# Kernel optimization log

Hardware: AMD Instinct MI355X
Metric: run time of the kernel (lower is better)

Reference implementation:

```python
import jax, jax.numpy as jnp
import numpy as np

THRESHOLD = 0.5
NEG_POS_RATIO = 3
CONF_WEIGHT = 1.0
VAR = (0.1, 0.1, 0.2, 0.2)
EPS_LOG = 1e-5


def _center_to_corner(p):
    cx, cy, w, h = p[:, 0], p[:, 1], p[:, 2], p[:, 3]
    return jnp.stack([cx - w / 2, cy - h / 2, cx + w / 2, cy + h / 2], axis=1)


def _iou(gt, pr):  # gt [M,4] corners, pr [P,4] corners -> [M,P]
    lt = jnp.maximum(gt[:, None, :2], pr[None, :, :2])
    rb = jnp.minimum(gt[:, None, 2:], pr[None, :, 2:])
    wh = jnp.clip(rb - lt, 0.0)
    inter = wh[..., 0] * wh[..., 1]
    area_g = (gt[:, 2] - gt[:, 0]) * (gt[:, 3] - gt[:, 1])
    area_p = (pr[:, 2] - pr[:, 0]) * (pr[:, 3] - pr[:, 1])
    return inter / (area_g[:, None] + area_p[None, :] - inter + 1e-10)


def _match_one(gt_boxes, priors_corner):
    # standard SSD matching: per-prior best GT if IoU >= threshold, else -1;
    # each GT additionally claims its best prior.
    iou = _iou(gt_boxes, priors_corner)            # [M,P]
    best_gt = jnp.argmax(iou, axis=0)              # [P]
    best_iou = jnp.max(iou, axis=0)                # [P]
    truth = jnp.where(best_iou >= THRESHOLD, best_gt, -1)
    best_prior = jnp.argmax(iou, axis=1)           # [M]
    truth = truth.at[best_prior].set(jnp.arange(gt_boxes.shape[0]))
    return truth


def _encode(matched_gt, priors):
    # matched_gt [B,P,4] corners, priors [P,4] center form -> [B,P,4]
    g_cx = (matched_gt[..., 0] + matched_gt[..., 2]) / 2
    g_cy = (matched_gt[..., 1] + matched_gt[..., 3]) / 2
    g_w = matched_gt[..., 2] - matched_gt[..., 0]
    g_h = matched_gt[..., 3] - matched_gt[..., 1]
    p_cx, p_cy, p_w, p_h = priors[:, 0], priors[:, 1], priors[:, 2], priors[:, 3]
    enc_cx = (g_cx - p_cx) / (p_w * VAR[0])
    enc_cy = (g_cy - p_cy) / (p_h * VAR[1])
    enc_w = jnp.log(g_w / p_w + EPS_LOG) / VAR[2]
    enc_h = jnp.log(g_h / p_h + EPS_LOG) / VAR[3]
    return jnp.stack([enc_cx, enc_cy, enc_w, enc_h], axis=-1)


def setup_inputs() -> dict:
    key = jax.random.key(0)
    ks = jax.random.split(key, 7)
    B, P, C, M = 64, 8732, 81, 20
    pred_loc = jax.random.normal(ks[0], (B, P, 4), jnp.float32)
    pred_conf = jax.random.normal(ks[1], (B, P, C), jnp.float32)
    # priors in center form (cx, cy, w, h)
    p_c = jax.random.uniform(ks[2], (P, 2), jnp.float32)
    p_wh = jax.random.uniform(ks[3], (P, 2), jnp.float32, minval=0.05, maxval=0.5)
    priors = jnp.concatenate([p_c, p_wh], axis=1)
    # GT boxes in corner form, guaranteed valid (x2>x1, y2>y1)
    g_c = jax.random.uniform(ks[4], (B, M, 2), jnp.float32, minval=0.2, maxval=0.8)
    g_wh = jax.random.uniform(ks[5], (B, M, 2), jnp.float32, minval=0.05, maxval=0.3)
    targets_boxes = jnp.concatenate([g_c - g_wh / 2, g_c + g_wh / 2], axis=-1)
    targets_labels = jax.random.randint(ks[6], (B, M), 1, C, jnp.int32)
    return {"pred_loc": pred_loc, "pred_conf": pred_conf, "priors": priors,
            "targets_boxes": targets_boxes, "targets_labels": targets_labels}


def reference(pred_loc, pred_conf, priors, targets_boxes, targets_labels):
    B, P, C = pred_conf.shape
    priors_corner = _center_to_corner(priors)
    truth = jax.vmap(lambda g: _match_one(g, priors_corner))(targets_boxes)  # [B,P]
    pos_mask = truth != -1
    safe = jnp.maximum(truth, 0)
    matched_gt = jax.vmap(lambda t, s: t[s])(targets_boxes, safe)            # [B,P,4]
    target_conf = jnp.where(pos_mask,
                            jax.vmap(lambda l, s: l[s])(targets_labels, safe), 0)

    # localization loss: smooth-L1 (beta=1), sum over matched priors, / batch
    enc = _encode(matched_gt, priors)
    d = pred_loc - enc
    ad = jnp.abs(d)
    sl1 = jnp.where(ad < 1.0, 0.5 * d * d, ad - 0.5)
    loc_loss = jnp.sum(sl1 * pos_mask[..., None]) / B

    # confidence loss with hard negative mining (3:1, double-argsort rank trick)
    logp = jax.nn.log_softmax(pred_conf, axis=-1)                            # [B,P,C]
    ce = -jnp.take_along_axis(logp, target_conf[..., None], axis=-1)[..., 0]  # [B,P]
    ce_neg = jnp.where(pos_mask, 0.0, ce)
    order = jnp.argsort(-ce_neg, axis=1)
    rank = jnp.argsort(order, axis=1)
    pos_num = jnp.sum(pos_mask, axis=1, keepdims=True)
    neg_num = jnp.minimum(NEG_POS_RATIO * pos_num, P - 1)
    neg_mask = rank < neg_num
    prior_mask = pos_mask | neg_mask
    conf_loss = jnp.sum(ce * prior_mask) / jnp.sum(prior_mask) / B * CONF_WEIGHT
    return (loc_loss, conf_loss)
```

## Files before the change

kernel.cpp:

```cpp
#include <hip/hip_runtime.h>
#include <hip/hip_bf16.h>

#define B_   64
#define P_   8732
#define C_   81
#define M_   20
#define BP_  (B_*P_)
#define NCH  9
#define CER  64
#define SBLK 1024

__global__ __launch_bounds__(256) void iou_kernel(
    const float* __restrict__ priors, const float* __restrict__ tboxes,
    int* __restrict__ truth, unsigned long long* __restrict__ bestc,
    int* __restrict__ pos_cnt, float* __restrict__ pos_sum,
    float* __restrict__ accums, int* __restrict__ done)
{
    const int b = blockIdx.y;
    const int tid = threadIdx.x;

    if (blockIdx.x == 0 && b == 0) {
        if (tid < B_) { pos_cnt[tid] = 0; pos_sum[tid] = 0.f; }
        if (tid >= B_ && tid < B_ + 3) accums[tid - B_] = 0.f;
        if (tid == B_ + 3) *done = 0;
    }

    __shared__ float s_gt[M_][4];
    __shared__ float s_ga[M_];
    __shared__ float s_red[M_][4];
    __shared__ int   s_redp[M_][4];

    if (tid < M_*4) ((float*)s_gt)[tid] = tboxes[b*M_*4 + tid];
    __syncthreads();
    if (tid < M_) s_ga[tid] = (s_gt[tid][2]-s_gt[tid][0]) * (s_gt[tid][3]-s_gt[tid][1]);
    __syncthreads();

    float lb[M_]; int lp[M_];
    #pragma unroll
    for (int m=0;m<M_;++m){ lb[m] = -1.0f; lp[m] = 0x7FFFFFFF; }

    const float4* pr4 = (const float4*)priors;
    const int p0 = blockIdx.x * 1024;
    const int pend = min(p0 + 1024, P_);
    for (int p = p0 + tid; p < pend; p += 256) {
        float4 pc = pr4[p];
        float px0 = pc.x - pc.z*0.5f, py0 = pc.y - pc.w*0.5f;
        float px1 = pc.x + pc.z*0.5f, py1 = pc.y + pc.w*0.5f;
        float pa = pc.z * pc.w;
        float best = -1.0f; int bg = 0;
        #pragma unroll
        for (int m=0;m<M_;++m){
            float ix0 = fmaxf(s_gt[m][0], px0);
            float iy0 = fmaxf(s_gt[m][1], py0);
            float ix1 = fminf(s_gt[m][2], px1);
            float iy1 = fminf(s_gt[m][3], py1);
            float iw = fmaxf(ix1-ix0, 0.f), ih = fmaxf(iy1-iy0, 0.f);
            float inter = iw*ih;
            float iou = inter / (s_ga[m] + pa - inter + 1e-10f);
            if (iou > best) { best = iou; bg = m; }
            if (iou > lb[m]) { lb[m] = iou; lp[m] = p; }
        }
        truth[(size_t)b*P_ + p] = (best >= 0.5f) ? bg : -1;
    }

    const int lane = tid & 63, wid = tid >> 6;
    #pragma unroll
    for (int m=0;m<M_;++m){
        float v = lb[m]; int ip = lp[m];
        for (int off=32; off; off>>=1){
            float ov = __shfl_down(v, off); int op = __shfl_down(ip, off);
            if (ov > v || (ov == v && op < ip)) { v = ov; ip = op; }
        }
        if (lane == 0) { s_red[m][wid] = v; s_redp[m][wid] = ip; }
    }
    __syncthreads();
    if (tid < M_) {
        const int m = tid;
        float v = s_red[m][0]; int ip = s_redp[m][0];
        for (int w=1; w<4; ++w){
            float ov = s_red[m][w]; int op = s_redp[m][w];
            if (ov > v || (ov == v && op < ip)) { v = ov; ip = op; }
        }
        bestc[(b*M_ + m)*NCH + blockIdx.x] =
            ((unsigned long long)__float_as_uint(v) << 32) | (unsigned)(P_ - 1 - ip);
    }
}

__global__ __launch_bounds__(256) void ce_loc_kernel(
    const float* __restrict__ pred_conf, const float* __restrict__ pred_loc,
    const float* __restrict__ priors, const float* __restrict__ tboxes,
    const int* __restrict__ tlabels, const int* __restrict__ truth,
    const unsigned long long* __restrict__ bestc,
    float* __restrict__ ce_neg, int* __restrict__ pos_cnt,
    float* __restrict__ pos_sum, float* __restrict__ accums)
{
    __shared__ int   s_fp[2][M_];
    __shared__ int   s_pos[2];
    __shared__ float s_psum[2];
    __shared__ float s_loc[4];
    const int tid = threadIdx.x;
    const int base = blockIdx.x * CER;
    const int b0 = base / P_;

    if (tid < 2*M_) {
        const int j = tid / M_, m = tid - j*M_;
        const int bb = b0 + j;
        int p = -1;
        if (bb < B_) {
            const unsigned long long* src = &bestc[(bb*M_ + m)*NCH];
            unsigned long long best = src[0];
            #pragma unroll
            for (int c = 1; c < NCH; ++c) { unsigned long long kk = src[c]; if (kk > best) best = kk; }
            p = P_ - 1 - (int)(unsigned)(best & 0xFFFFFFFFu);
        }
        s_fp[j][m] = p;
    }
    if (tid < 2) { s_pos[tid] = 0; s_psum[tid] = 0.f; }
    __syncthreads();

    const int r = tid >> 2;
    const int q = tid & 3;
    const int bp = base + r;
    const int b  = bp / P_;
    const int p  = bp - b * P_;
    const int jb = b - b0;
    const float* row = pred_conf + (size_t)bp * C_;

    float v[21];
    #pragma unroll
    for (int i = 0; i < 21; ++i) {
        const int c = q + 4*i;
        v[i] = (c < C_) ? row[c] : -1e30f;
    }
    float mx = v[0];
    #pragma unroll
    for (int i = 1; i < 21; ++i) mx = fmaxf(mx, v[i]);
    mx = fmaxf(mx, __shfl_xor(mx, 1));
    mx = fmaxf(mx, __shfl_xor(mx, 2));
    float s = 0.f;
    #pragma unroll
    for (int i = 0; i < 21; ++i) s += __expf(v[i] - mx);
    s += __shfl_xor(s, 1);
    s += __shfl_xor(s, 2);

    float locacc = 0.f;
    if (q == 0) {
        int t = truth[bp];
        #pragma unroll
        for (int m = 0; m < M_; ++m)
            if (s_fp[jb][m] == p) t = m;
        const int cls = (t >= 0) ? tlabels[b*M_ + t] : 0;
        const float ce = mx + __logf(s) - row[cls];
        if (t >= 0) {
            atomicAdd(&s_pos[jb], 1);
            atomicAdd(&s_psum[jb], ce);
            ce_neg[bp] = 0.f;
            float4 pc = ((const float4*)priors)[p];
            float4 g  = ((const float4*)tboxes)[b*M_ + t];
            float gcx = (g.x+g.z)*0.5f, gcy = (g.y+g.w)*0.5f;
            float gw = g.z - g.x, gh = g.w - g.y;
            float e0 = (gcx - pc.x) / (pc.z * 0.1f);
            float e1 = (gcy - pc.y) / (pc.w * 0.1f);
            float e2 = __logf(gw / pc.z + 1e-5f) * 5.0f;
            float e3 = __logf(gh / pc.w + 1e-5f) * 5.0f;
            float4 pl = ((const float4*)pred_loc)[bp];
            float d0 = pl.x-e0, d1 = pl.y-e1, d2 = pl.z-e2, d3 = pl.w-e3;
            float a0 = fabsf(d0), a1 = fabsf(d1), a2 = fabsf(d2), a3 = fabsf(d3);
            locacc = (a0<1.f ? 0.5f*d0*d0 : a0-0.5f)
                   + (a1<1.f ? 0.5f*d1*d1 : a1-0.5f)
                   + (a2<1.f ? 0.5f*d2*d2 : a2-0.5f)
                   + (a3<1.f ? 0.5f*d3*d3 : a3-0.5f);
        } else {
            ce_neg[bp] = ce;
        }
    }

    for (int off=32; off; off>>=1) locacc += __shfl_down(locacc, off);
    if ((tid & 63) == 0) s_loc[tid>>6] = locacc;
    __syncthreads();
    if (tid == 0) {
        float a = s_loc[0]+s_loc[1]+s_loc[2]+s_loc[3];
        if (a != 0.f) atomicAdd(&accums[0], a);
    }
    if (tid < 2) {
        const int br = b0 + tid;
        if (br < B_ && s_pos[tid] > 0) {
            atomicAdd(&pos_cnt[br], s_pos[tid]);
            atomicAdd(&pos_sum[br], s_psum[tid]);
        }
    }
}

__global__ __launch_bounds__(SBLK) void select_kernel(
    const float* __restrict__ ce_neg, const int* __restrict__ pos_cnt,
    const float* __restrict__ pos_sum, float* __restrict__ accums,
    int* __restrict__ done, float* __restrict__ out)
{
    const int b = blockIdx.x; const int tid = threadIdx.x;
    const int lane = tid & 63;
    __shared__ float cl[P_];
    __shared__ unsigned hist[256];
    __shared__ unsigned s_sel, s_prefix, s_remk, s_cntgt;
    __shared__ float s_r1[SBLK/64];
    __shared__ int s_last;

    const float* cerow = ce_neg + (size_t)b * P_;
    if (tid < 256) hist[tid] = 0u;
    if (tid == 0) s_sel = 0u;
    __syncthreads();

    for (int i = tid; i < P_; i += SBLK) {
        const unsigned bin = __float_as_uint(cerow[i]) >> 24;
        unsigned long long todo = __ballot(1);
        while (todo) {
            const int src = (int)__ffsll(todo) - 1;
            const unsigned lead = __shfl(bin, src);
            const unsigned long long mset = __ballot(bin == lead);
            if (lane == src) atomicAdd(&hist[lead], (unsigned)__popcll(mset));
            todo &= ~mset;
        }
    }
    __syncthreads();
    const int pos = pos_cnt[b];
    const unsigned k = (unsigned)min(3 * pos, P_ - 1);
    if (tid == 0) {
        unsigned acc = 0, chosen = 0;
        for (int bin = 255; bin >= 0; --bin) {
            const unsigned c = hist[bin];
            if (acc + c >= k) { chosen = (unsigned)bin; break; }
            acc += c;
        }
        s_prefix = chosen << 24; s_remk = k - acc; s_cntgt = acc;
    }
    __syncthreads();
    const unsigned c3 = s_prefix >> 24;

    float gsum = 0.f;
    for (int i = tid; i < P_; i += SBLK) {
        const float v = cerow[i];
        const unsigned byt = __float_as_uint(v) >> 24;
        if (byt > c3) gsum += v;
        const bool pred = (byt == c3);
        const unsigned long long mset = __ballot(pred);
        if (pred) {
            const int leader = (int)__ffsll(mset) - 1;
            unsigned bse;
            if (lane == leader) bse = atomicAdd(&s_sel, (unsigned)__popcll(mset));
            bse = __shfl(bse, leader);
            cl[bse + __popcll(mset & ((1ull << lane) - 1ull))] = v;
        }
    }
    __syncthreads();
    const int L = (int)s_sel;

    for (int pass = 2; pass >= 0; --pass) {
        if (tid < 256) hist[tid] = 0u;
        __syncthreads();
        const unsigned prefix = s_prefix;
        const int shift = pass * 8;
        const unsigned pmask = 0xFFFFFFFFu << (shift + 8);
        for (int i = tid; i < L; i += SBLK) {
            const unsigned u = __float_as_uint(cl[i]);
            if ((u & pmask) == prefix) atomicAdd(&hist[(u >> shift) & 0xFFu], 1u);
        }
        __syncthreads();
        if (tid == 0) {
            unsigned remk = s_remk, acc = 0, chosen = 0;
            for (int bin = 255; bin >= 0; --bin) {
                const unsigned c = hist[bin];
                if (acc + c >= remk) { chosen = (unsigned)bin; break; }
                acc += c;
            }
            s_cntgt += acc; s_remk = remk - acc; s_prefix = prefix | (chosen << shift);
        }
        __syncthreads();
    }

    const unsigned Tbits = s_prefix;
    const float T = __uint_as_float(Tbits);
    float sgt = gsum;
    for (int i = tid; i < L; i += SBLK) {
        const float v = cl[i];
        if (__float_as_uint(v) > Tbits) sgt += v;
    }
    for (int off=32; off; off>>=1) sgt += __shfl_down(sgt, off);
    if (lane == 0) s_r1[tid>>6] = sgt;
    __syncthreads();
    if (tid == 0) {
        float a = 0.f;
        #pragma unroll
        for (int w = 0; w < SBLK/64; ++w) a += s_r1[w];
        const unsigned sel_eq = s_remk;
        float neg_sum, mc;
        if (Tbits != 0u) { neg_sum = a + (float)sel_eq * T; mc = (float)(pos + (int)k); }
        else             { neg_sum = a;                     mc = (float)(pos + (int)s_cntgt); }
        atomicAdd(&accums[1], pos_sum[b] + neg_sum);
        atomicAdd(&accums[2], mc);
        __threadfence();
        const int old = atomicAdd(done, 1);
        s_last = (old == B_ - 1);
    }
    __syncthreads();
    if (tid == 0 && s_last) {
        const float l  = atomicAdd(&accums[0], 0.f);
        const float cs = atomicAdd(&accums[1], 0.f);
        const float mn = atomicAdd(&accums[2], 0.f);
        out[0] = l / (float)B_;
        out[1] = cs / mn / (float)B_;
    }
}

extern "C" void kernel_launch(void* const* d_in, const int* in_sizes, int n_in,
                              void* d_out, int out_size, void* d_ws, size_t ws_size,
                              hipStream_t stream) {
    (void)in_sizes; (void)n_in; (void)out_size; (void)ws_size;
    const float* pred_loc  = (const float*)d_in[0];
    const float* pred_conf = (const float*)d_in[1];
    const float* priors    = (const float*)d_in[2];
    const float* tboxes    = (const float*)d_in[3];
    const int*   tlabels   = (const int*)d_in[4];
    float* out = (float*)d_out;

    char* ws = (char*)d_ws;
    int*   truth  = (int*)ws;
    float* ce_neg = (float*)(ws + (size_t)BP_ * 4);
    unsigned long long* bestc = (unsigned long long*)(ws + (size_t)BP_ * 8);
    char* tail = ws + (size_t)BP_ * 8 + (size_t)B_*M_*NCH*8;
    int*   pos_cnt = (int*)tail;
    float* pos_sum = (float*)(tail + B_*4);
    float* accums  = (float*)(tail + B_*8);
    int*   done    = (int*)(tail + B_*8 + 12);

    iou_kernel<<<dim3(NCH, B_), 256, 0, stream>>>(priors, tboxes, truth, bestc,
                                                  pos_cnt, pos_sum, accums, done);
    ce_loc_kernel<<<BP_ / CER, 256, 0, stream>>>(pred_conf, pred_loc, priors, tboxes,
                                                 tlabels, truth, bestc,
                                                 ce_neg, pos_cnt, pos_sum, accums);
    select_kernel<<<B_, SBLK, 0, stream>>>(ce_neg, pos_cnt, pos_sum, accums, done, out);
}
```

Baseline: 187.2 us.

## Process three softmax rows per wavefront with contiguous vector loads

```diff
diff --git a/kernel.cpp b/kernel.cpp
--- a/kernel.cpp
+++ b/kernel.cpp
@@ -7,8 +7,13 @@
 #define M_   20
 #define BP_  (B_*P_)
 #define NCH  9
-#define CER  64
 #define SBLK 1024
+#define GRPS ((BP_ + 2) / 3)
+#define CENB ((GRPS + 3) / 4)
+#define DWT  (BP_ * 81)
+
+typedef float floatx4 __attribute__((ext_vector_type(4)));
+typedef floatx4 __attribute__((aligned(4))) floatx4_u;
 
 __global__ __launch_bounds__(256) void iou_kernel(
     const float* __restrict__ priors, const float* __restrict__ tboxes,
@@ -99,84 +104,119 @@
     __shared__ float s_psum[2];
     __shared__ float s_loc[4];
     const int tid = threadIdx.x;
-    const int base = blockIdx.x * CER;
+    const int base = blockIdx.x * 12;
     const int b0 = base / P_;
 
     if (tid < 2*M_) {
         const int j = tid / M_, m = tid - j*M_;
         const int bb = b0 + j;
-        int p = -1;
+        int pp = -1;
         if (bb < B_) {
             const unsigned long long* src = &bestc[(bb*M_ + m)*NCH];
             unsigned long long best = src[0];
             #pragma unroll
             for (int c = 1; c < NCH; ++c) { unsigned long long kk = src[c]; if (kk > best) best = kk; }
-            p = P_ - 1 - (int)(unsigned)(best & 0xFFFFFFFFu);
-        }
-        s_fp[j][m] = p;
+            pp = P_ - 1 - (int)(unsigned)(best & 0xFFFFFFFFu);
+        }
+        s_fp[j][m] = pp;
     }
     if (tid < 2) { s_pos[tid] = 0; s_psum[tid] = 0.f; }
     __syncthreads();
 
-    const int r = tid >> 2;
-    const int q = tid & 3;
-    const int bp = base + r;
-    const int b  = bp / P_;
-    const int p  = bp - b * P_;
-    const int jb = b - b0;
-    const float* row = pred_conf + (size_t)bp * C_;
-
-    float v[21];
+    const int w = tid >> 6, lane = tid & 63;
+    const int grp = blockIdx.x * 4 + w;
+    const int gd  = grp * 243;
+    const int ld  = gd + 4*lane;
+    const int lcl = min(ld, DWT - 4);
+
+    floatx4 t = *(const floatx4_u*)(pred_conf + lcl);
+    float a0 = t.x, a1 = t.y, a2 = t.z, a3 = t.w;
+    asm volatile("" : "+v"(a0), "+v"(a1), "+v"(a2), "+v"(a3));
+
+    const int d0 = 4*lane;
+    const float x0 = ((d0+0 < 243) && (ld+0 < DWT)) ? a0 : -1e30f;
+    const float x1 = ((d0+1 < 243) && (ld+1 < DWT)) ? a1 : -1e30f;
+    const float x2 = ((d0+2 < 243) && (ld+2 < DWT)) ? a2 : -1e30f;
+    const float x3 = ((d0+3 < 243) && (ld+3 < DWT)) ? a3 : -1e30f;
+
+    float m0=-1e30f, m1=-1e30f, m2=-1e30f;
+    m0 = (d0+0 <  81) ? fmaxf(m0,x0) : m0;
+    m1 = (d0+0 >= 81 && d0+0 < 162) ? fmaxf(m1,x0) : m1;
+    m2 = (d0+0 >= 162) ? fmaxf(m2,x0) : m2;
+    m0 = (d0+1 <  81) ? fmaxf(m0,x1) : m0;
+    m1 = (d0+1 >= 81 && d0+1 < 162) ? fmaxf(m1,x1) : m1;
+    m2 = (d0+1 >= 162) ? fmaxf(m2,x1) : m2;
+    m0 = (d0+2 <  81) ? fmaxf(m0,x2) : m0;
+    m1 = (d0+2 >= 81 && d0+2 < 162) ? fmaxf(m1,x2) : m1;
+    m2 = (d0+2 >= 162) ? fmaxf(m2,x2) : m2;
+    m0 = (d0+3 <  81) ? fmaxf(m0,x3) : m0;
+    m1 = (d0+3 >= 81 && d0+3 < 162) ? fmaxf(m1,x3) : m1;
+    m2 = (d0+3 >= 162) ? fmaxf(m2,x3) : m2;
     #pragma unroll
-    for (int i = 0; i < 21; ++i) {
-        const int c = q + 4*i;
-        v[i] = (c < C_) ? row[c] : -1e30f;
-    }
-    float mx = v[0];
+    for (int off=32; off; off>>=1) {
+        m0 = fmaxf(m0, __shfl_xor(m0, off));
+        m1 = fmaxf(m1, __shfl_xor(m1, off));
+        m2 = fmaxf(m2, __shfl_xor(m2, off));
+    }
+
+    float s0=0.f, s1=0.f, s2=0.f;
+    {
+        const float e0 = __expf(x0 - ((d0+0<81)?m0:((d0+0<162)?m1:m2)));
+        const float e1 = __expf(x1 - ((d0+1<81)?m0:((d0+1<162)?m1:m2)));
+        const float e2 = __expf(x2 - ((d0+2<81)?m0:((d0+2<162)?m1:m2)));
+        const float e3 = __expf(x3 - ((d0+3<81)?m0:((d0+3<162)?m1:m2)));
+        s0 += (d0+0<81)?e0:0.f; s1 += (d0+0>=81&&d0+0<162)?e0:0.f; s2 += (d0+0>=162)?e0:0.f;
+        s0 += (d0+1<81)?e1:0.f; s1 += (d0+1>=81&&d0+1<162)?e1:0.f; s2 += (d0+1>=162)?e1:0.f;
+        s0 += (d0+2<81)?e2:0.f; s1 += (d0+2>=81&&d0+2<162)?e2:0.f; s2 += (d0+2>=162)?e2:0.f;
+        s0 += (d0+3<81)?e3:0.f; s1 += (d0+3>=81&&d0+3<162)?e3:0.f; s2 += (d0+3>=162)?e3:0.f;
+    }
     #pragma unroll
-    for (int i = 1; i < 21; ++i) mx = fmaxf(mx, v[i]);
-    mx = fmaxf(mx, __shfl_xor(mx, 1));
-    mx = fmaxf(mx, __shfl_xor(mx, 2));
-    float s = 0.f;
-    #pragma unroll
-    for (int i = 0; i < 21; ++i) s += __expf(v[i] - mx);
-    s += __shfl_xor(s, 1);
-    s += __shfl_xor(s, 2);
+    for (int off=32; off; off>>=1) {
+        s0 += __shfl_xor(s0, off);
+        s1 += __shfl_xor(s1, off);
+        s2 += __shfl_xor(s2, off);
+    }
 
     float locacc = 0.f;
-    if (q == 0) {
-        int t = truth[bp];
+    const int rg = grp*3 + lane;
+    if (lane < 3 && rg < BP_) {
+        const float mx   = (lane==0) ? m0 : ((lane==1) ? m1 : m2);
+        const float ssum = (lane==0) ? s0 : ((lane==1) ? s1 : s2);
+        const int b  = rg / P_;
+        const int p  = rg - b*P_;
+        const int jb = b - b0;
+        int t2 = truth[rg];
         #pragma unroll
         for (int m = 0; m < M_; ++m)
-            if (s_fp[jb][m] == p) t = m;
-        const int cls = (t >= 0) ? tlabels[b*M_ + t] : 0;
-        const float ce = mx + __logf(s) - row[cls];
-        if (t >= 0) {
+            if (s_fp[jb][m] == p) t2 = m;
+        const int cls = (t2 >= 0) ? tlabels[b*M_ + t2] : 0;
+        const float ce = mx + __logf(ssum) - pred_conf[(size_t)rg*C_ + cls];
+        if (t2 >= 0) {
             atomicAdd(&s_pos[jb], 1);
             atomicAdd(&s_psum[jb], ce);
-            ce_neg[bp] = 0.f;
+            ce_neg[rg] = 0.f;
             float4 pc = ((const float4*)priors)[p];
-            float4 g  = ((const float4*)tboxes)[b*M_ + t];
+            float4 g  = ((const float4*)tboxes)[b*M_ + t2];
             float gcx = (g.x+g.z)*0.5f, gcy = (g.y+g.w)*0.5f;
             float gw = g.z - g.x, gh = g.w - g.y;
             float e0 = (gcx - pc.x) / (pc.z * 0.1f);
             float e1 = (gcy - pc.y) / (pc.w * 0.1f);
             float e2 = __logf(gw / pc.z + 1e-5f) * 5.0f;
             float e3 = __logf(gh / pc.w + 1e-5f) * 5.0f;
-            float4 pl = ((const float4*)pred_loc)[bp];
-            float d0 = pl.x-e0, d1 = pl.y-e1, d2 = pl.z-e2, d3 = pl.w-e3;
-            float a0 = fabsf(d0), a1 = fabsf(d1), a2 = fabsf(d2), a3 = fabsf(d3);
-            locacc = (a0<1.f ? 0.5f*d0*d0 : a0-0.5f)
-                   + (a1<1.f ? 0.5f*d1*d1 : a1-0.5f)
-                   + (a2<1.f ? 0.5f*d2*d2 : a2-0.5f)
-                   + (a3<1.f ? 0.5f*d3*d3 : a3-0.5f);
+            float4 pl = ((const float4*)pred_loc)[rg];
+            float d0_ = pl.x-e0, d1_ = pl.y-e1, d2_ = pl.z-e2, d3_ = pl.w-e3;
+            float a0_ = fabsf(d0_), a1_ = fabsf(d1_), a2_ = fabsf(d2_), a3_ = fabsf(d3_);
+            locacc = (a0_<1.f ? 0.5f*d0_*d0_ : a0_-0.5f)
+                   + (a1_<1.f ? 0.5f*d1_*d1_ : a1_-0.5f)
+                   + (a2_<1.f ? 0.5f*d2_*d2_ : a2_-0.5f)
+                   + (a3_<1.f ? 0.5f*d3_*d3_ : a3_-0.5f);
         } else {
-            ce_neg[bp] = ce;
+            ce_neg[rg] = ce;
         }
     }
 
     for (int off=32; off; off>>=1) locacc += __shfl_down(locacc, off);
-    if ((tid & 63) == 0) s_loc[tid>>6] = locacc;
+    if (lane == 0) s_loc[w] = locacc;
     __syncthreads();
     if (tid == 0) {
         float a = s_loc[0]+s_loc[1]+s_loc[2]+s_loc[3];
@@ -333,8 +373,8 @@
 
     iou_kernel<<<dim3(NCH, B_), 256, 0, stream>>>(priors, tboxes, truth, bestc,
                                                   pos_cnt, pos_sum, accums, done);
-    ce_loc_kernel<<<BP_ / CER, 256, 0, stream>>>(pred_conf, pred_loc, priors, tboxes,
-                                                 tlabels, truth, bestc,
-                                                 ce_neg, pos_cnt, pos_sum, accums);
+    ce_loc_kernel<<<CENB, 256, 0, stream>>>(pred_conf, pred_loc, priors, tboxes,
+                                            tlabels, truth, bestc,
+                                            ce_neg, pos_cnt, pos_sum, accums);
     select_kernel<<<B_, SBLK, 0, stream>>>(ce_neg, pos_cnt, pos_sum, accums, done, out);
 }
```

After: 258.5 us. 1.38x slower.
